# Kernel optimization log

Hardware: AMD Instinct MI355X
Metric: run time of the kernel (lower is better)

## Reference

```python
import jax, jax.numpy as jnp
import numpy as np

GRID_SIZE = 8
SPLINE_ORDER = 3
LAYERS = [256, 512, 512, 256]  # [input_dim] + hidden_dims
BATCH = 8192
BN_EPS = 1e-5


def make_grid(in_features):
    # efficient-kan/torchkan grid: uniform on [-1, 1] extended by spline_order on each side
    h = 2.0 / GRID_SIZE
    g = jnp.arange(-SPLINE_ORDER, GRID_SIZE + SPLINE_ORDER + 1, dtype=jnp.float32) * h - 1.0
    return jnp.broadcast_to(g, (in_features, g.shape[0]))  # (In, G + 2k + 1)


def b_splines(x, grid):
    # x: (B, In), grid: (In, G + 2k + 1) -> bases: (B, In, G + k)
    xg = x[:, :, None]
    bases = ((xg >= grid[:, :-1]) & (xg < grid[:, 1:])).astype(x.dtype)
    for k in range(1, SPLINE_ORDER + 1):
        left = (xg - grid[:, : -(k + 1)]) / (grid[:, k:-1] - grid[:, : -(k + 1)])
        right = (grid[:, k + 1 :] - xg) / (grid[:, k + 1 :] - grid[:, 1:-k])
        bases = left * bases[:, :, :-1] + right * bases[:, :, 1:]
    return bases


def kan_linear(x, grid, base_w, spline_w):
    # base path: GELU (exact, matching torch.nn.GELU) then linear
    base_out = jax.nn.gelu(x, approximate=False) @ base_w.T
    spline_out = jnp.einsum('bik,oik->bo', b_splines(x, grid), spline_w)
    return base_out + spline_out


def setup_inputs() -> dict:
    key = jax.random.key(0)
    ks = jax.random.split(key, 16)
    inp = {'x': jax.random.normal(ks[0], (BATCH, LAYERS[0]), dtype=jnp.float32)}
    n_bases = GRID_SIZE + SPLINE_ORDER
    for i, (fin, fout) in enumerate(zip(LAYERS[:-1], LAYERS[1:])):
        scale = 1.0 / np.sqrt(fin)
        inp[f'grid{i}'] = make_grid(fin)
        inp[f'base_w{i}'] = jax.random.normal(ks[1 + 3 * i], (fout, fin), dtype=jnp.float32) * scale
        inp[f'spline_w{i}'] = jax.random.normal(ks[2 + 3 * i], (fout, fin, n_bases), dtype=jnp.float32) * (0.1 * scale)
    d_out = LAYERS[-1]
    inp['bn_gamma'] = jnp.ones((d_out,), dtype=jnp.float32)
    inp['bn_beta'] = jnp.zeros((d_out,), dtype=jnp.float32)
    inp['bn_mean'] = jax.random.normal(ks[10], (d_out,), dtype=jnp.float32) * 0.1
    inp['bn_var'] = jax.random.uniform(ks[11], (d_out,), dtype=jnp.float32, minval=0.5, maxval=1.5)
    return inp


def reference(x, grid0, base_w0, spline_w0, grid1, base_w1, spline_w1, grid2, base_w2, spline_w2, bn_gamma, bn_beta, bn_mean, bn_var):
    h = kan_linear(x, grid0, base_w0, spline_w0)
    h = kan_linear(h, grid1, base_w1, spline_w1)
    h = kan_linear(h, grid2, base_w2, spline_w2)
    # BatchNorm1d in eval mode (running stats); Dropout is identity at inference
    return bn_gamma * (h - bn_mean) * jax.lax.rsqrt(bn_var + BN_EPS) + bn_beta
```

## Files before the change

kernel.cpp:

```cpp
#include <hip/hip_runtime.h>
#include <hip/hip_bf16.h>
#include <cstdint>


typedef unsigned short ushort_t;
typedef __bf16 bf16x8 __attribute__((ext_vector_type(8)));
typedef float f32x4 __attribute__((ext_vector_type(4)));

__device__ __forceinline__ ushort_t f2bf(float f) {
    __bf16 h = (__bf16)f;
    return __builtin_bit_cast(ushort_t, h);
}

__device__ __forceinline__ void gload_lds16(const void* g, void* lds) {
    __builtin_amdgcn_global_load_lds(
        (const __attribute__((address_space(1))) unsigned int*)(uintptr_t)g,
        (__attribute__((address_space(3))) unsigned int*)(unsigned int)(uintptr_t)lds,
        16, 0, 0);
}

__device__ __forceinline__ void expand12(float x, ushort_t* o) {
    float x3 = x * x * x;
    float y  = 0.7978845608028654f * (x + 0.044715f * x3);
    float e  = __expf(2.0f * y);
    float th = 1.0f - 2.0f / (e + 1.0f);
    o[0] = f2bf(0.5f * x * (1.0f + th));
    float xs = (x + 1.75f) * 4.0f;
#pragma unroll
    for (int j = 0; j < 11; ++j) {
        float t  = xs - (float)j;
        float a  = fabsf(t - 2.0f);
        float p1 = (3.0f * a - 6.0f) * a * a + 4.0f;
        float c  = 2.0f - a;
        float p2 = c * c * c;
        float v  = (a <= 1.0f) ? p1 : fmaxf(p2, 0.0f);
        o[1 + j] = f2bf(v * (1.0f / 6.0f));
    }
}

template <bool SUM>
__global__ __launch_bounds__(256) void expand_kernel(
    const float* __restrict__ X0, const float* __restrict__ X1,
    ushort_t* __restrict__ A, int total2)
{
    int idx = blockIdx.x * 256 + threadIdx.x;
    if (idx >= total2) return;
    float2 h = *(const float2*)(X0 + 2 * (size_t)idx);
    if (SUM) {
        float2 h2 = *(const float2*)(X1 + 2 * (size_t)idx);
        h.x += h2.x; h.y += h2.y;
    }
    union { ushort_t us[24]; uint4 v[3]; } pk;
    expand12(h.x, pk.us);
    expand12(h.y, pk.us + 12);
    uint4* dst = (uint4*)(A + (size_t)idx * 24);
    dst[0] = pk.v[0]; dst[1] = pk.v[1]; dst[2] = pk.v[2];
}

__global__ __launch_bounds__(256) void pack_w_kernel(
    const float* __restrict__ bw, const float* __restrict__ sw,
    ushort_t* __restrict__ W, int total)
{
    int idx = blockIdx.x * 256 + threadIdx.x;
    if (idx >= total) return;
    union { ushort_t us[12]; uint2 v[3]; } pk;
    pk.us[0] = f2bf(bw[idx]);
    const float* s = sw + (size_t)idx * 11;
#pragma unroll
    for (int k = 0; k < 11; ++k) pk.us[1 + k] = f2bf(s[k]);
    uint2* dst = (uint2*)(W + (size_t)idx * 12);
    dst[0] = pk.v[0]; dst[1] = pk.v[1]; dst[2] = pk.v[2];
}

#define SLOT 24576
#define ASZ  8192

__global__ __launch_bounds__(512, 2) void gemm_kernel(
    const ushort_t* __restrict__ A,
    const ushort_t* __restrict__ W,
    float* __restrict__ C,
    int M, int N, int K, int kcps)
{
    extern __shared__ __align__(16) ushort_t lds[];

    const int t   = threadIdx.x;
    const int l   = t & 63;
    const int w   = t >> 6;
    const int wm  = w >> 2;
    const int wn  = w & 3;
    const int l15 = l & 15;
    const int q   = l >> 4;
    const int blockM = blockIdx.x * 128;
    const int blockN = blockIdx.y * 256;
    const int kb0 = blockIdx.z * kcps;
    const int nt  = kcps;
    float* Cz = C + (size_t)blockIdx.z * M * N;

    const ushort_t* Ab = A + (size_t)blockM * K;
    const ushort_t* Wb = W + (size_t)blockN * K;

    auto stage_a = [&](int kb, ushort_t* dst) {
#pragma unroll
        for (int it = 0; it < 2; ++it) {
            int s   = it * 512 + t;
            int row = s >> 3, c = s & 7;
            int g   = c ^ (row & 7);
            gload_lds16(Ab + ((size_t)row * K + (kb << 6) + g * 8), dst + s * 8);
        }
    };
    auto stage_b = [&](int kb, ushort_t* dst, int half) {
#pragma unroll
        for (int it = 0; it < 2; ++it) {
            int s   = (half * 2 + it) * 512 + t;
            int row = s >> 3, c = s & 7;
            int g   = c ^ (row & 7);
            gload_lds16(Wb + ((size_t)row * K + (kb << 6) + g * 8), dst + s * 8);
        }
    };

    f32x4 acc[4][4];
#pragma unroll
    for (int i = 0; i < 4; ++i)
#pragma unroll
        for (int j = 0; j < 4; ++j) acc[i][j] = (f32x4){0.f, 0.f, 0.f, 0.f};

    stage_a(kb0, lds);            stage_b(kb0, lds + ASZ, 0);       stage_b(kb0, lds + ASZ, 1);
    stage_a(kb0 + 1, lds + SLOT); stage_b(kb0 + 1, lds + SLOT + ASZ, 0);
    stage_b(kb0 + 1, lds + SLOT + ASZ, 1);
    asm volatile("s_waitcnt vmcnt(6)" ::: "memory");
    __builtin_amdgcn_s_barrier();

    int cur = 0;
    for (int tt = 0; tt < nt; ++tt) {
        ushort_t* Ac = lds + cur * SLOT;
        ushort_t* Bc = Ac + ASZ;
        int nx = cur + 2; if (nx >= 3) nx -= 3;
        ushort_t* An = lds + nx * SLOT;
        ushort_t* Bn = An + ASZ;
        const bool pre = (tt + 2 < nt);
        const int  kbp = kb0 + tt + 2;

        bf16x8 af[2], bf[4];

        if (pre) stage_a(kbp, An);
        {
            const int kc = q;
#pragma unroll
            for (int ni = 0; ni < 4; ++ni) {
                int n = wn * 64 + ni * 16 + l15;
                bf[ni] = *(const bf16x8*)&Bc[(n * 8 + (kc ^ (n & 7))) * 8];
            }
#pragma unroll
            for (int mi = 0; mi < 2; ++mi) {
                int m = wm * 64 + mi * 16 + l15;
                af[mi] = *(const bf16x8*)&Ac[(m * 8 + (kc ^ (m & 7))) * 8];
            }
        }
        __builtin_amdgcn_s_barrier();
        asm volatile("s_waitcnt lgkmcnt(0)" ::: "memory");
        __builtin_amdgcn_s_setprio(1);
#pragma unroll
        for (int mi = 0; mi < 2; ++mi)
#pragma unroll
            for (int ni = 0; ni < 4; ++ni)
                acc[mi][ni] = __builtin_amdgcn_mfma_f32_16x16x32_bf16(
                    af[mi], bf[ni], acc[mi][ni], 0, 0, 0);
        __builtin_amdgcn_s_setprio(0);
        __builtin_amdgcn_s_barrier();

        if (pre) stage_b(kbp, Bn, 0);
        {
            const int kc = q;
#pragma unroll
            for (int mi = 0; mi < 2; ++mi) {
                int m = wm * 64 + (mi + 2) * 16 + l15;
                af[mi] = *(const bf16x8*)&Ac[(m * 8 + (kc ^ (m & 7))) * 8];
            }
        }
        __builtin_amdgcn_s_barrier();
        asm volatile("s_waitcnt lgkmcnt(0)" ::: "memory");
        __builtin_amdgcn_s_setprio(1);
#pragma unroll
        for (int mi = 0; mi < 2; ++mi)
#pragma unroll
            for (int ni = 0; ni < 4; ++ni)
                acc[mi + 2][ni] = __builtin_amdgcn_mfma_f32_16x16x32_bf16(
                    af[mi], bf[ni], acc[mi + 2][ni], 0, 0, 0);
        __builtin_amdgcn_s_setprio(0);
        __builtin_amdgcn_s_barrier();

        if (pre) stage_b(kbp, Bn, 1);
        {
            const int kc = 4 + q;
#pragma unroll
            for (int ni = 0; ni < 4; ++ni) {
                int n = wn * 64 + ni * 16 + l15;
                bf[ni] = *(const bf16x8*)&Bc[(n * 8 + (kc ^ (n & 7))) * 8];
            }
#pragma unroll
            for (int mi = 0; mi < 2; ++mi) {
                int m = wm * 64 + mi * 16 + l15;
                af[mi] = *(const bf16x8*)&Ac[(m * 8 + (kc ^ (m & 7))) * 8];
            }
        }
        __builtin_amdgcn_s_barrier();
        asm volatile("s_waitcnt lgkmcnt(0)" ::: "memory");
        __builtin_amdgcn_s_setprio(1);
#pragma unroll
        for (int mi = 0; mi < 2; ++mi)
#pragma unroll
            for (int ni = 0; ni < 4; ++ni)
                acc[mi][ni] = __builtin_amdgcn_mfma_f32_16x16x32_bf16(
                    af[mi], bf[ni], acc[mi][ni], 0, 0, 0);
        __builtin_amdgcn_s_setprio(0);
        __builtin_amdgcn_s_barrier();

        {
            const int kc = 4 + q;
#pragma unroll
            for (int mi = 0; mi < 2; ++mi) {
                int m = wm * 64 + (mi + 2) * 16 + l15;
                af[mi] = *(const bf16x8*)&Ac[(m * 8 + (kc ^ (m & 7))) * 8];
            }
        }
        __builtin_amdgcn_s_barrier();
        asm volatile("s_waitcnt lgkmcnt(0)" ::: "memory");
        __builtin_amdgcn_s_setprio(1);
#pragma unroll
        for (int mi = 0; mi < 2; ++mi)
#pragma unroll
            for (int ni = 0; ni < 4; ++ni)
                acc[mi + 2][ni] = __builtin_amdgcn_mfma_f32_16x16x32_bf16(
                    af[mi], bf[ni], acc[mi + 2][ni], 0, 0, 0);
        __builtin_amdgcn_s_setprio(0);
        if (pre) asm volatile("s_waitcnt vmcnt(6)" ::: "memory");
        else     asm volatile("s_waitcnt vmcnt(0)" ::: "memory");
        __builtin_amdgcn_s_barrier();

        cur = cur + 1; if (cur == 3) cur = 0;
    }

#pragma unroll
    for (int ni = 0; ni < 4; ++ni) {
        int n = blockN + wn * 64 + ni * 16 + l15;
#pragma unroll
        for (int mi = 0; mi < 4; ++mi) {
            int mb = blockM + wm * 64 + mi * 16 + q * 4;
#pragma unroll
            for (int r = 0; r < 4; ++r)
                Cz[(size_t)(mb + r) * N + n] = acc[mi][ni][r];
        }
    }
}

__global__ __launch_bounds__(256) void bn_reduce_kernel(
    const float4* __restrict__ Q0, const float4* __restrict__ Q1,
    const float4* __restrict__ Q2, const float4* __restrict__ Q3,
    const float* __restrict__ gamma, const float* __restrict__ beta,
    const float* __restrict__ mean,  const float* __restrict__ var,
    float4* __restrict__ out, int n4)
{
    int i = blockIdx.x * 256 + threadIdx.x;
    if (i >= n4) return;
    float4 a = Q0[i], b = Q1[i], c = Q2[i], d = Q3[i];
    int nb = (i * 4) & 255;
    float4 g  = *(const float4*)(gamma + nb);
    float4 be = *(const float4*)(beta + nb);
    float4 mn = *(const float4*)(mean + nb);
    float4 vr = *(const float4*)(var + nb);
    float4 o;
    o.x = g.x * rsqrtf(vr.x + 1e-5f) * (a.x + b.x + c.x + d.x - mn.x) + be.x;
    o.y = g.y * rsqrtf(vr.y + 1e-5f) * (a.y + b.y + c.y + d.y - mn.y) + be.y;
    o.z = g.z * rsqrtf(vr.z + 1e-5f) * (a.z + b.z + c.z + d.z - mn.z) + be.z;
    o.w = g.w * rsqrtf(vr.w + 1e-5f) * (a.w + b.w + c.w + d.w - mn.w) + be.w;
    out[i] = o;
}

extern "C" void kernel_launch(void* const* d_in, const int* in_sizes, int n_in,
                              void* d_out, int out_size, void* d_ws, size_t ws_size,
                              hipStream_t stream) {
    const float* x     = (const float*)d_in[0];
    const float* bw0   = (const float*)d_in[2];
    const float* sw0   = (const float*)d_in[3];
    const float* bw1   = (const float*)d_in[5];
    const float* sw1   = (const float*)d_in[6];
    const float* bw2   = (const float*)d_in[8];
    const float* sw2   = (const float*)d_in[9];
    const float* gamma = (const float*)d_in[10];
    const float* beta  = (const float*)d_in[11];
    const float* mean  = (const float*)d_in[12];
    const float* var   = (const float*)d_in[13];

    char* ws = (char*)d_ws;
    ushort_t* Abuf = (ushort_t*)(ws);
    ushort_t* W0   = (ushort_t*)(ws + 100663296);
    ushort_t* W1   = (ushort_t*)(ws + 103809024);
    ushort_t* W2   = (ushort_t*)(ws + 110100480);
    float*    P0   = (float*)(ws + 113246208);
    float*    P1   = (float*)(ws + 130023424);
    float*    Q0   = (float*)(ws + 113246208);
    float*    Q1   = (float*)(ws + 121634816);
    float*    Q2   = (float*)(ws + 130023424);
    float*    Q3   = (float*)(ws + 138412032);
    float*    out  = (float*)d_out;

    const size_t GEMM_LDS = 3 * SLOT * sizeof(ushort_t);

    pack_w_kernel<<<(512 * 256 + 255) / 256, 256, 0, stream>>>(bw0, sw0, W0, 512 * 256);
    pack_w_kernel<<<(512 * 512 + 255) / 256, 256, 0, stream>>>(bw1, sw1, W1, 512 * 512);
    pack_w_kernel<<<(256 * 512 + 255) / 256, 256, 0, stream>>>(bw2, sw2, W2, 256 * 512);

    expand_kernel<false><<<4096, 256, 0, stream>>>(x, nullptr, Abuf, 8192 * 256 / 2);
    {
        dim3 g(64, 2, 2);
        gemm_kernel<<<g, 512, GEMM_LDS, stream>>>(Abuf, W0, P0, 8192, 512, 3072, 24);
    }
    expand_kernel<true><<<8192, 256, 0, stream>>>(P0, P1, Abuf, 8192 * 512 / 2);
    {
        dim3 g(64, 2, 2);
        gemm_kernel<<<g, 512, GEMM_LDS, stream>>>(Abuf, W1, P0, 8192, 512, 6144, 48);
    }
    expand_kernel<true><<<8192, 256, 0, stream>>>(P0, P1, Abuf, 8192 * 512 / 2);
    {
        dim3 g(64, 1, 4);
        gemm_kernel<<<g, 512, GEMM_LDS, stream>>>(Abuf, W2, Q0, 8192, 256, 6144, 24);
    }
    bn_reduce_kernel<<<2048, 256, 0, stream>>>(
        (const float4*)Q0, (const float4*)Q1, (const float4*)Q2, (const float4*)Q3,
        gamma, beta, mean, var, (float4*)out, 8192 * 256 / 4);
}
```

Before: 303.9 us.

## Split GEMM K-tile across wave groups and reduce partials through LDS

Reorganises the 8 waves of the GEMM block from a 2x4 M-by-N grid into 4 N-waves times 2 K-groups. Each wave now computes the full 128-row by 64-column tile over half of each 64-wide K chunk. The old four barrier-separated MFMA phases per iteration collapse into one fragment load and one MFMA burst. Partial sums are combined through a padded LDS buffer at the end. This aims to cut barriers and LDS fragment reloads. In exchange it doubles the accumulator registers to 128 per lane under a 2-blocks-per-CU launch bound, which risks spilling or lower occupancy, and it adds an epilogue reduction.

```diff
diff --git a/kernel.cpp b/kernel.cpp
--- a/kernel.cpp
+++ b/kernel.cpp
@@ -85,9 +85,8 @@
 
     const int t   = threadIdx.x;
     const int l   = t & 63;
-    const int w   = t >> 6;
-    const int wm  = w >> 2;
-    const int wn  = w & 3;
+    const int wn  = (t >> 6) & 3;
+    const int kg  = t >> 8;
     const int l15 = l & 15;
     const int q   = l >> 4;
     const int blockM = blockIdx.x * 128;
@@ -108,131 +107,62 @@
             gload_lds16(Ab + ((size_t)row * K + (kb << 6) + g * 8), dst + s * 8);
         }
     };
-    auto stage_b = [&](int kb, ushort_t* dst, int half) {
-#pragma unroll
-        for (int it = 0; it < 2; ++it) {
-            int s   = (half * 2 + it) * 512 + t;
+    auto stage_b = [&](int kb, ushort_t* dst) {
+#pragma unroll
+        for (int it = 0; it < 4; ++it) {
+            int s   = it * 512 + t;
             int row = s >> 3, c = s & 7;
             int g   = c ^ (row & 7);
             gload_lds16(Wb + ((size_t)row * K + (kb << 6) + g * 8), dst + s * 8);
         }
     };
 
-    f32x4 acc[4][4];
-#pragma unroll
-    for (int i = 0; i < 4; ++i)
+    f32x4 acc[8][4];
+#pragma unroll
+    for (int i = 0; i < 8; ++i)
 #pragma unroll
         for (int j = 0; j < 4; ++j) acc[i][j] = (f32x4){0.f, 0.f, 0.f, 0.f};
 
-    stage_a(kb0, lds);            stage_b(kb0, lds + ASZ, 0);       stage_b(kb0, lds + ASZ, 1);
-    stage_a(kb0 + 1, lds + SLOT); stage_b(kb0 + 1, lds + SLOT + ASZ, 0);
-    stage_b(kb0 + 1, lds + SLOT + ASZ, 1);
+    stage_a(kb0, lds);            stage_b(kb0, lds + ASZ);
+    stage_a(kb0 + 1, lds + SLOT); stage_b(kb0 + 1, lds + SLOT + ASZ);
     asm volatile("s_waitcnt vmcnt(6)" ::: "memory");
     __builtin_amdgcn_s_barrier();
 
+    const int kc = kg * 4 + q;
     int cur = 0;
     for (int tt = 0; tt < nt; ++tt) {
         ushort_t* Ac = lds + cur * SLOT;
         ushort_t* Bc = Ac + ASZ;
         int nx = cur + 2; if (nx >= 3) nx -= 3;
-        ushort_t* An = lds + nx * SLOT;
-        ushort_t* Bn = An + ASZ;
         const bool pre = (tt + 2 < nt);
-        const int  kbp = kb0 + tt + 2;
-
-        bf16x8 af[2], bf[4];
-
-        if (pre) stage_a(kbp, An);
-        {
-            const int kc = q;
-#pragma unroll
-            for (int ni = 0; ni < 4; ++ni) {
-                int n = wn * 64 + ni * 16 + l15;
-                bf[ni] = *(const bf16x8*)&Bc[(n * 8 + (kc ^ (n & 7))) * 8];
-            }
-#pragma unroll
-            for (int mi = 0; mi < 2; ++mi) {
-                int m = wm * 64 + mi * 16 + l15;
-                af[mi] = *(const bf16x8*)&Ac[(m * 8 + (kc ^ (m & 7))) * 8];
-            }
-        }
-        __builtin_amdgcn_s_barrier();
-        asm volatile("s_waitcnt lgkmcnt(0)" ::: "memory");
+
+        if (pre) {
+            ushort_t* An = lds + nx * SLOT;
+            stage_a(kb0 + tt + 2, An);
+            stage_b(kb0 + tt + 2, An + ASZ);
+        }
+
+        bf16x8 bfr[4], afr[8];
+#pragma unroll
+        for (int ni = 0; ni < 4; ++ni) {
+            int n = wn * 64 + ni * 16 + l15;
+            bfr[ni] = *(const bf16x8*)&Bc[(size_t)(n * 8 + (kc ^ (n & 7))) * 8];
+        }
+#pragma unroll
+        for (int mi = 0; mi < 8; ++mi) {
+            int m = mi * 16 + l15;
+            afr[mi] = *(const bf16x8*)&Ac[(size_t)(m * 8 + (kc ^ (m & 7))) * 8];
+        }
         __builtin_amdgcn_s_setprio(1);
 #pragma unroll
-        for (int mi = 0; mi < 2; ++mi)
+        for (int mi = 0; mi < 8; ++mi)
 #pragma unroll
             for (int ni = 0; ni < 4; ++ni)
                 acc[mi][ni] = __builtin_amdgcn_mfma_f32_16x16x32_bf16(
-                    af[mi], bf[ni], acc[mi][ni], 0, 0, 0);
+                    afr[mi], bfr[ni], acc[mi][ni], 0, 0, 0);
         __builtin_amdgcn_s_setprio(0);
-        __builtin_amdgcn_s_barrier();
-
-        if (pre) stage_b(kbp, Bn, 0);
-        {
-            const int kc = q;
-#pragma unroll
-            for (int mi = 0; mi < 2; ++mi) {
-                int m = wm * 64 + (mi + 2) * 16 + l15;
-                af[mi] = *(const bf16x8*)&Ac[(m * 8 + (kc ^ (m & 7))) * 8];
-            }
-        }
-        __builtin_amdgcn_s_barrier();
+
         asm volatile("s_waitcnt lgkmcnt(0)" ::: "memory");
-        __builtin_amdgcn_s_setprio(1);
-#pragma unroll
-        for (int mi = 0; mi < 2; ++mi)
-#pragma unroll
-            for (int ni = 0; ni < 4; ++ni)
-                acc[mi + 2][ni] = __builtin_amdgcn_mfma_f32_16x16x32_bf16(
-                    af[mi], bf[ni], acc[mi + 2][ni], 0, 0, 0);
-        __builtin_amdgcn_s_setprio(0);
-        __builtin_amdgcn_s_barrier();
-
-        if (pre) stage_b(kbp, Bn, 1);
-        {
-            const int kc = 4 + q;
-#pragma unroll
-            for (int ni = 0; ni < 4; ++ni) {
-                int n = wn * 64 + ni * 16 + l15;
-                bf[ni] = *(const bf16x8*)&Bc[(n * 8 + (kc ^ (n & 7))) * 8];
-            }
-#pragma unroll
-            for (int mi = 0; mi < 2; ++mi) {
-                int m = wm * 64 + mi * 16 + l15;
-                af[mi] = *(const bf16x8*)&Ac[(m * 8 + (kc ^ (m & 7))) * 8];
-            }
-        }
-        __builtin_amdgcn_s_barrier();
-        asm volatile("s_waitcnt lgkmcnt(0)" ::: "memory");
-        __builtin_amdgcn_s_setprio(1);
-#pragma unroll
-        for (int mi = 0; mi < 2; ++mi)
-#pragma unroll
-            for (int ni = 0; ni < 4; ++ni)
-                acc[mi][ni] = __builtin_amdgcn_mfma_f32_16x16x32_bf16(
-                    af[mi], bf[ni], acc[mi][ni], 0, 0, 0);
-        __builtin_amdgcn_s_setprio(0);
-        __builtin_amdgcn_s_barrier();
-
-        {
-            const int kc = 4 + q;
-#pragma unroll
-            for (int mi = 0; mi < 2; ++mi) {
-                int m = wm * 64 + (mi + 2) * 16 + l15;
-                af[mi] = *(const bf16x8*)&Ac[(m * 8 + (kc ^ (m & 7))) * 8];
-            }
-        }
-        __builtin_amdgcn_s_barrier();
-        asm volatile("s_waitcnt lgkmcnt(0)" ::: "memory");
-        __builtin_amdgcn_s_setprio(1);
-#pragma unroll
-        for (int mi = 0; mi < 2; ++mi)
-#pragma unroll
-            for (int ni = 0; ni < 4; ++ni)
-                acc[mi + 2][ni] = __builtin_amdgcn_mfma_f32_16x16x32_bf16(
-                    af[mi], bf[ni], acc[mi + 2][ni], 0, 0, 0);
-        __builtin_amdgcn_s_setprio(0);
         if (pre) asm volatile("s_waitcnt vmcnt(6)" ::: "memory");
         else     asm volatile("s_waitcnt vmcnt(0)" ::: "memory");
         __builtin_amdgcn_s_barrier();
@@ -240,15 +170,34 @@
         cur = cur + 1; if (cur == 3) cur = 0;
     }
 
-#pragma unroll
-    for (int ni = 0; ni < 4; ++ni) {
-        int n = blockN + wn * 64 + ni * 16 + l15;
-#pragma unroll
-        for (int mi = 0; mi < 4; ++mi) {
-            int mb = blockM + wm * 64 + mi * 16 + q * 4;
-#pragma unroll
-            for (int r = 0; r < 4; ++r)
-                Cz[(size_t)(mb + r) * N + n] = acc[mi][ni][r];
+    float* ldsf = (float*)lds;
+    if (kg == 1) {
+#pragma unroll
+        for (int mi = 0; mi < 8; ++mi)
+#pragma unroll
+            for (int ni = 0; ni < 4; ++ni) {
+                int col = wn * 64 + ni * 16 + l15;
+#pragma unroll
+                for (int r = 0; r < 4; ++r)
+                    ldsf[(size_t)(mi * 16 + q * 4 + r) * 257 + col] = acc[mi][ni][r];
+            }
+    }
+    __syncthreads();
+    if (kg == 0) {
+#pragma unroll
+        for (int ni = 0; ni < 4; ++ni) {
+            int col = wn * 64 + ni * 16 + l15;
+            int n   = blockN + col;
+#pragma unroll
+            for (int mi = 0; mi < 8; ++mi) {
+                int mb = blockM + mi * 16 + q * 4;
+#pragma unroll
+                for (int r = 0; r < 4; ++r) {
+                    float v = acc[mi][ni][r] +
+                              ldsf[(size_t)(mi * 16 + q * 4 + r) * 257 + col];
+                    Cz[(size_t)(mb + r) * N + n] = v;
+                }
+            }
         }
     }
 }
```

Result: faster. 297.3 us (-2.2%).
